# Performance work log

Hardware: AMD Instinct MI355X
Metric: run time of the kernel (lower is better)

## Reference

```python
import jax, jax.numpy as jnp
import numpy as np

N = 50000          # nodes
E = 1600000        # edges (avg degree 32)
D_MODEL = 128      # input == output dim
HEADS = 4
D_HEAD = D_MODEL // HEADS
N_LAYERS = 3


def _edge_softmax(scores, dst, n):
    # scores: [E, H]; softmax over edges sharing the same destination node
    m = jax.ops.segment_max(scores, dst, num_segments=n)          # [N, H]
    m = jnp.where(jnp.isfinite(m), m, 0.0)                        # empty segments -> -inf guard
    ex = jnp.exp(scores - m[dst])                                 # [E, H]
    denom = jax.ops.segment_sum(ex, dst, num_segments=n)          # [N, H]
    return ex / (denom[dst] + 1e-9)


def _gt_layer(h, src, dst, Wq, Wk, Wv, Wo):
    # h: [N, D]; one multi-head graph-attention (graph transformer) layer
    n = h.shape[0]
    q = (h @ Wq).reshape(n, HEADS, D_HEAD)
    k = (h @ Wk).reshape(n, HEADS, D_HEAD)
    v = (h @ Wv).reshape(n, HEADS, D_HEAD)
    scale = 1.0 / np.sqrt(D_HEAD).astype(np.float32)
    scores = jnp.einsum('ehd,ehd->eh', q[dst], k[src]) * scale    # [E, H]
    alpha = _edge_softmax(scores, dst, n)                         # [E, H]
    agg = jax.ops.segment_sum(alpha[:, :, None] * v[src], dst, num_segments=n)  # [N, H, Dh]
    return agg.reshape(n, D_MODEL) @ Wo


def setup_inputs() -> dict:
    key = jax.random.key(0)
    ks = jax.random.split(key, 16)
    s = 1.0 / np.sqrt(D_MODEL)
    inp = {
        'X':    jax.random.normal(ks[0], (N, 1), jnp.float32),
        'Seed': jax.random.uniform(ks[1], (N, 1), jnp.float32),
        'D':    jax.random.uniform(ks[2], (N, 1), jnp.float32),
        'C':    jax.random.uniform(ks[3], (N, 1), jnp.float32),
        'edge_src': jax.random.randint(ks[4], (E,), 0, N, jnp.int32),
        'edge_dst': jax.random.randint(ks[5], (E,), 0, N, jnp.int32),
        # scalar -> d_model embeddings (Linear(1, d, bias=False))
        'W_seed': jax.random.normal(ks[6], (1, D_MODEL), jnp.float32),
        'W_deg':  jax.random.normal(ks[7], (1, D_MODEL), jnp.float32),
        'W_clu':  jax.random.normal(ks[8], (1, D_MODEL), jnp.float32),
        # 3 graph-transformer layers
        'Wq': jax.random.normal(ks[9],  (N_LAYERS, D_MODEL, D_MODEL), jnp.float32) * s,
        'Wk': jax.random.normal(ks[10], (N_LAYERS, D_MODEL, D_MODEL), jnp.float32) * s,
        'Wv': jax.random.normal(ks[11], (N_LAYERS, D_MODEL, D_MODEL), jnp.float32) * s,
        'Wo': jax.random.normal(ks[12], (N_LAYERS, D_MODEL, D_MODEL), jnp.float32) * s,
        # MLP head: Linear(d,d)+ReLU, Linear(d,1)
        'W1': jax.random.normal(ks[13], (D_MODEL, D_MODEL), jnp.float32) * s,
        'b1': jnp.zeros((D_MODEL,), jnp.float32),
        'W2': jax.random.normal(ks[14], (D_MODEL, 1), jnp.float32) * s,
        'b2': jnp.zeros((1,), jnp.float32),
    }
    return inp


def reference(X, Seed, D, C, edge_src, edge_dst,
              W_seed, W_deg, W_clu, Wq, Wk, Wv, Wo, W1, b1, W2, b2):
    # faithful to original: raw X [N,1] broadcast-added to the embeddings
    h = X + Seed @ W_seed + D @ W_deg + C @ W_clu                 # [N, D_MODEL]
    for i in range(N_LAYERS):
        h = _gt_layer(h, edge_src, edge_dst, Wq[i], Wk[i], Wv[i], Wo[i])
    z = jax.nn.relu(h @ W1 + b1)
    return z @ W2 + b2                                            # [N, 1]
```

## Files before the change

### kernel.cpp

```cpp
#include <hip/hip_runtime.h>
#include <math.h>

#define DM 128
#define HEADS 4
#define DH 32
#define WSTRIDE 16384

typedef _Float16 f16x8 __attribute__((ext_vector_type(8)));
typedef _Float16 f16x4 __attribute__((ext_vector_type(4)));
typedef _Float16 f16x2 __attribute__((ext_vector_type(2)));
typedef float f32x4v __attribute__((ext_vector_type(4)));

__device__ __forceinline__ float dpp_xor1_add(float x) {
    int r = __builtin_amdgcn_update_dpp(0, __builtin_bit_cast(int, x), 0xB1, 0xf, 0xf, true);
    return x + __builtin_bit_cast(float, r);
}
__device__ __forceinline__ float dpp_xor2_add(float x) {
    int r = __builtin_amdgcn_update_dpp(0, __builtin_bit_cast(int, x), 0x4E, 0xf, 0xf, true);
    return x + __builtin_bit_cast(float, r);
}
__device__ __forceinline__ uint32_t pkh(float x, float y) {
    f16x2 h = {(_Float16)x, (_Float16)y};
    return __builtin_bit_cast(uint32_t, h);
}

__global__ void count_kernel(const int* __restrict__ edst, int* __restrict__ deg, int E) {
    int e = blockIdx.x * blockDim.x + threadIdx.x;
    if (e < E) atomicAdd(&deg[edst[e]], 1);
}

__global__ void scan1_kernel(const int* __restrict__ in, int* __restrict__ outv,
                             int* __restrict__ bsums, int n) {
    __shared__ int s[256];
    int t = threadIdx.x;
    int i = blockIdx.x * 256 + t;
    int v = (i < n) ? in[i] : 0;
    s[t] = v;
    __syncthreads();
    for (int off = 1; off < 256; off <<= 1) {
        int x = (t >= off) ? s[t - off] : 0;
        __syncthreads();
        s[t] += x;
        __syncthreads();
    }
    if (i < n) outv[i] = s[t];
    if (t == 255) bsums[blockIdx.x] = s[255];
}

__global__ void scan2_kernel(int* __restrict__ bsums, int nb) {
    __shared__ int s[256];
    int t = threadIdx.x;
    int v = (t < nb) ? bsums[t] : 0;
    s[t] = v;
    __syncthreads();
    for (int off = 1; off < 256; off <<= 1) {
        int x = (t >= off) ? s[t - off] : 0;
        __syncthreads();
        s[t] += x;
        __syncthreads();
    }
    if (t < nb) bsums[t] = s[t];
}

__global__ void scan3_kernel(const int* __restrict__ outv, const int* __restrict__ bsums,
                             int* __restrict__ ptr, int n) {
    int i = blockIdx.x * 256 + threadIdx.x;
    if (i == 0) ptr[0] = 0;
    if (i < n) {
        int add = (blockIdx.x > 0) ? bsums[blockIdx.x - 1] : 0;
        ptr[i + 1] = outv[i] + add;
    }
}

__global__ void scatter_kernel(const int* __restrict__ esrc, const int* __restrict__ edst,
                               const int* __restrict__ ptr, int* __restrict__ fill,
                               int* __restrict__ out, int E) {
    int e = blockIdx.x * blockDim.x + threadIdx.x;
    if (e >= E) return;
    int d = edst[e];
    int pos = ptr[d] + atomicAdd(&fill[d], 1);
    out[pos] = esrc[e];
}

__global__ void prepack_kernel(const float* __restrict__ Wq, const float* __restrict__ Wk,
                               const float* __restrict__ Wv, const float* __restrict__ Wo,
                               const float* __restrict__ W1, _Float16* __restrict__ W16) {
    int m = blockIdx.z;
    const float* W;
    if (m < 3)       W = Wq + (size_t)m * DM * DM;
    else if (m < 6)  W = Wk + (size_t)(m - 3) * DM * DM;
    else if (m < 9)  W = Wv + (size_t)(m - 6) * DM * DM;
    else if (m < 12) W = Wo + (size_t)(m - 9) * DM * DM;
    else             W = W1;
    int kb = blockIdx.x, nb = blockIdx.y, l = threadIdx.x;
    int kbase = kb * 32 + (l >> 4) * 8;
    int c = nb * 16 + (l & 15);
    f16x8 v;
#pragma unroll
    for (int j = 0; j < 8; j++) v[j] = (_Float16)W[(kbase + j) * DM + c];
    *reinterpret_cast<f16x8*>(W16 + (size_t)m * WSTRIDE + ((kb * 8 + nb) * 64 + l) * 8) = v;
}

__device__ __forceinline__ void tile_gemm(const _Float16* __restrict__ sRow,
                                          const _Float16* __restrict__ W16, int lg, int l,
                                          f32x4v acc[8]) {
#pragma unroll
    for (int nb = 0; nb < 8; nb++) acc[nb] = (f32x4v){0.f, 0.f, 0.f, 0.f};
#pragma unroll
    for (int kb = 0; kb < 4; kb++) {
        f16x8 a = *reinterpret_cast<const f16x8*>(sRow + kb * 32 + lg * 8);
#pragma unroll
        for (int nb = 0; nb < 8; nb++) {
            f16x8 b = *reinterpret_cast<const f16x8*>(&W16[((kb * 8 + nb) * 64 + l) * 8]);
            acc[nb] = __builtin_amdgcn_mfma_f32_16x16x32_f16(a, b, acc[nb], 0, 0, 0);
        }
    }
}

__device__ __forceinline__ void qkv_store(const _Float16* __restrict__ sH, int rowb, int lr,
                                          int lg, int l, int row0, int n,
                                          const _Float16* __restrict__ Wq16,
                                          const _Float16* __restrict__ Wk16,
                                          const _Float16* __restrict__ Wv16,
                                          _Float16* __restrict__ Qo,
                                          _Float16* __restrict__ KVo) {
    const _Float16* sRow = sH + (rowb + lr) * 136;
    f32x4v acc[8];
    tile_gemm(sRow, Wq16, lg, l, acc);
#pragma unroll
    for (int nb = 0; nb < 8; nb++)
#pragma unroll
        for (int i = 0; i < 4; i++) {
            int r = row0 + rowb + lg * 4 + i;
            if (r < n) Qo[(size_t)r * DM + nb * 16 + lr] = (_Float16)acc[nb][i];
        }
    tile_gemm(sRow, Wk16, lg, l, acc);
#pragma unroll
    for (int nb = 0; nb < 8; nb++)
#pragma unroll
        for (int i = 0; i < 4; i++) {
            int r = row0 + rowb + lg * 4 + i;
            if (r < n) KVo[(size_t)r * 256 + nb * 16 + lr] = (_Float16)acc[nb][i];
        }
    tile_gemm(sRow, Wv16, lg, l, acc);
#pragma unroll
    for (int nb = 0; nb < 8; nb++)
#pragma unroll
        for (int i = 0; i < 4; i++) {
            int r = row0 + rowb + lg * 4 + i;
            if (r < n) KVo[(size_t)r * 256 + 128 + nb * 16 + lr] = (_Float16)acc[nb][i];
        }
}

__global__ __launch_bounds__(256) void fused_embed_qkv_kernel(
    const float* __restrict__ X, const float* __restrict__ Seed,
    const float* __restrict__ Dg, const float* __restrict__ Cl,
    const float* __restrict__ Wseed, const float* __restrict__ Wdeg,
    const float* __restrict__ Wclu,
    const _Float16* __restrict__ Wq16, const _Float16* __restrict__ Wk16,
    const _Float16* __restrict__ Wv16,
    _Float16* __restrict__ Qo, _Float16* __restrict__ KVo, int n) {
    __shared__ _Float16 sH[64 * 136];
    int t = threadIdx.x;
    int row0 = blockIdx.x * 64;
    {
        int row = t >> 2, qt = t & 3;
        int gr = min(row0 + row, n - 1);
        float x = X[gr], sd = Seed[gr], dg = Dg[gr], cl = Cl[gr];
#pragma unroll
        for (int j = 0; j < 8; j++) {
            int c4 = qt * 32 + j * 4;
            float4 ws = *reinterpret_cast<const float4*>(Wseed + c4);
            float4 wd = *reinterpret_cast<const float4*>(Wdeg + c4);
            float4 wc = *reinterpret_cast<const float4*>(Wclu + c4);
            f16x4 h;
            h[0] = (_Float16)(x + sd * ws.x + dg * wd.x + cl * wc.x);
            h[1] = (_Float16)(x + sd * ws.y + dg * wd.y + cl * wc.y);
            h[2] = (_Float16)(x + sd * ws.z + dg * wd.z + cl * wc.z);
            h[3] = (_Float16)(x + sd * ws.w + dg * wd.w + cl * wc.w);
            *reinterpret_cast<f16x4*>(&sH[row * 136 + c4]) = h;
        }
    }
    __syncthreads();
    int w = t >> 6, l = t & 63;
    qkv_store(sH, w * 16, l & 15, l >> 4, l, row0, n, Wq16, Wk16, Wv16, Qo, KVo);
}

__global__ __launch_bounds__(256) void fused_wo_qkv_kernel(
    const _Float16* __restrict__ Ain, const _Float16* __restrict__ Wo16,
    const _Float16* __restrict__ Wq16, const _Float16* __restrict__ Wk16,
    const _Float16* __restrict__ Wv16,
    _Float16* __restrict__ Qo, _Float16* __restrict__ KVo, int n) {
    __shared__ _Float16 sA[64 * 136];
    __shared__ _Float16 sH[64 * 136];
    int t = threadIdx.x;
    int row0 = blockIdx.x * 64;
#pragma unroll
    for (int p = 0; p < 4; p++) {
        int f = p * 256 + t;
        int r = f >> 4, c8 = (f & 15) * 8;
        int gr = min(row0 + r, n - 1);
        *reinterpret_cast<uint4*>(&sA[r * 136 + c8]) =
            *reinterpret_cast<const uint4*>(Ain + (size_t)gr * DM + c8);
    }
    __syncthreads();
    int w = t >> 6, l = t & 63;
    int lr = l & 15, lg = l >> 4;
    int rowb = w * 16;
    f32x4v acc[8];
    tile_gemm(sA + (rowb + lr) * 136, Wo16, lg, l, acc);
#pragma unroll
    for (int nb = 0; nb < 8; nb++)
#pragma unroll
        for (int i = 0; i < 4; i++)
            sH[(rowb + lg * 4 + i) * 136 + nb * 16 + lr] = (_Float16)acc[nb][i];
    __syncthreads();
    qkv_store(sH, rowb, lr, lg, l, row0, n, Wq16, Wk16, Wv16, Qo, KVo);
}

__global__ __launch_bounds__(256) void fused_wo_mlp_kernel(
    const _Float16* __restrict__ Ain, const _Float16* __restrict__ Wo16,
    const _Float16* __restrict__ W116, const float* __restrict__ b1,
    const float* __restrict__ W2, const float* __restrict__ b2,
    float* __restrict__ out, int n) {
    __shared__ _Float16 sA[64 * 136];
    __shared__ _Float16 sH[64 * 136];
    int t = threadIdx.x;
    int row0 = blockIdx.x * 64;
#pragma unroll
    for (int p = 0; p < 4; p++) {
        int f = p * 256 + t;
        int r = f >> 4, c8 = (f & 15) * 8;
        int gr = min(row0 + r, n - 1);
        *reinterpret_cast<uint4*>(&sA[r * 136 + c8]) =
            *reinterpret_cast<const uint4*>(Ain + (size_t)gr * DM + c8);
    }
    __syncthreads();
    int w = t >> 6, l = t & 63;
    int lr = l & 15, lg = l >> 4;
    int rowb = w * 16;
    f32x4v acc[8];
    tile_gemm(sA + (rowb + lr) * 136, Wo16, lg, l, acc);
#pragma unroll
    for (int nb = 0; nb < 8; nb++)
#pragma unroll
        for (int i = 0; i < 4; i++)
            sH[(rowb + lg * 4 + i) * 136 + nb * 16 + lr] = (_Float16)acc[nb][i];
    __syncthreads();
    tile_gemm(sH + (rowb + lr) * 136, W116, lg, l, acc);
    float part[4] = {0.f, 0.f, 0.f, 0.f};
#pragma unroll
    for (int nb = 0; nb < 8; nb++) {
        int c = nb * 16 + lr;
        float b1v = b1[c];
        float w2v = W2[c];
#pragma unroll
        for (int i = 0; i < 4; i++) {
            float z = fmaxf(acc[nb][i] + b1v, 0.f);
            part[i] += z * w2v;
        }
    }
    float b2v = b2[0];
#pragma unroll
    for (int i = 0; i < 4; i++) {
        part[i] += __shfl_xor(part[i], 1, 64);
        part[i] += __shfl_xor(part[i], 2, 64);
        part[i] += __shfl_xor(part[i], 4, 64);
        part[i] += __shfl_xor(part[i], 8, 64);
        int r = row0 + rowb + lg * 4 + i;
        if (lr == 0 && r < n) out[r] = part[i] + b2v;
    }
}

__global__ __launch_bounds__(256) void attn_kernel(const _Float16* __restrict__ Q,
                                                   const uint32_t* __restrict__ KV,
                                                   const int* __restrict__ ptr,
                                                   const int* __restrict__ esrc,
                                                   _Float16* __restrict__ AGG, int n) {
    int wv = threadIdx.x >> 6;
    int lane = threadIdx.x & 63;
    int node = blockIdx.x * 4 + wv;
    if (node >= n) return;
    int e0 = ptr[node], e1 = ptr[node + 1];
    int q4 = lane >> 4;
    int w = lane & 15;
    _Float16* outbase = AGG + (size_t)node * DM + 8 * w;
    if (e0 >= e1) {
        if (lane < 16) *reinterpret_cast<uint4*>(outbase) = make_uint4(0, 0, 0, 0);
        return;
    }
    const float scale = 0.17677669529663687f * 1.4426950408889634f;
    uint4 qv = *reinterpret_cast<const uint4*>(Q + (size_t)node * DM + 8 * w);
    f16x2 qh0 = __builtin_bit_cast(f16x2, qv.x);
    f16x2 qh1 = __builtin_bit_cast(f16x2, qv.y);
    f16x2 qh2 = __builtin_bit_cast(f16x2, qv.z);
    f16x2 qh3 = __builtin_bit_cast(f16x2, qv.w);

    float m = -1e30f, s = 0.f;
    float a0 = 0.f, a1 = 0.f, a2 = 0.f, a3 = 0.f, a4 = 0.f, a5 = 0.f, a6 = 0.f, a7 = 0.f;

    int last = e1 - 1;
    int niter = (e1 - e0 + 3) >> 2;
    int niter2 = (niter + 1) >> 1;

    const uint32_t* kvw = KV + w * 4;

    uint4 k0, v0, k1, v1;
    {
        int i0 = esrc[min(e0 + q4, last)];
        const uint32_t* r0 = kvw + (size_t)i0 * 128;
        k0 = *reinterpret_cast<const uint4*>(r0);
        v0 = *reinterpret_cast<const uint4*>(r0 + 64);
        int i1 = esrc[min(e0 + 4 + q4, last)];
        const uint32_t* r1 = kvw + (size_t)i1 * 128;
        k1 = *reinterpret_cast<const uint4*>(r1);
        v1 = *reinterpret_cast<const uint4*>(r1 + 64);
    }
    int idx2 = esrc[min(e0 + 8 + q4, last)];

#define APROC(kc, vc, bidx)                                                            \
    {                                                                                  \
        float p = __builtin_amdgcn_fdot2(qh0, __builtin_bit_cast(f16x2, (kc).x), 0.f, false); \
        p = __builtin_amdgcn_fdot2(qh1, __builtin_bit_cast(f16x2, (kc).y), p, false);  \
        p = __builtin_amdgcn_fdot2(qh2, __builtin_bit_cast(f16x2, (kc).z), p, false);  \
        p = __builtin_amdgcn_fdot2(qh3, __builtin_bit_cast(f16x2, (kc).w), p, false);  \
        p = dpp_xor1_add(p);                                                           \
        p = dpp_xor2_add(p);                                                           \
        p *= scale;                                                                    \
        p = ((bidx) < e1) ? p : -3.0e38f;                                              \
        float diff = p - m;                                                            \
        if (__any(diff > 8.f)) {                                                       \
            float mn = fmaxf(m, p);                                                    \
            float dd = exp2f(m - mn);                                                  \
            s *= dd;                                                                   \
            a0 *= dd; a1 *= dd; a2 *= dd; a3 *= dd;                                    \
            a4 *= dd; a5 *= dd; a6 *= dd; a7 *= dd;                                    \
            m = mn;                                                                    \
            diff = p - m;                                                              \
        }                                                                              \
        float wg = exp2f(diff);                                                        \
        s += wg;                                                                       \
        f16x2 vh0 = __builtin_bit_cast(f16x2, (vc).x);                                 \
        f16x2 vh1 = __builtin_bit_cast(f16x2, (vc).y);                                 \
        f16x2 vh2 = __builtin_bit_cast(f16x2, (vc).z);                                 \
        f16x2 vh3 = __builtin_bit_cast(f16x2, (vc).w);                                 \
        a0 += wg * (float)vh0[0]; a1 += wg * (float)vh0[1];                            \
        a2 += wg * (float)vh1[0]; a3 += wg * (float)vh1[1];                            \
        a4 += wg * (float)vh2[0]; a5 += wg * (float)vh2[1];                            \
        a6 += wg * (float)vh3[0]; a7 += wg * (float)vh3[1];                            \
    }

    int b = e0 + q4;
    for (int it = 0; it < niter2; it++) {
        {
            uint4 kc = k0, vc = v0;
            const uint32_t* r = kvw + (size_t)idx2 * 128;
            k0 = *reinterpret_cast<const uint4*>(r);
            v0 = *reinterpret_cast<const uint4*>(r + 64);
            idx2 = esrc[min(b + 12, last)];
            APROC(kc, vc, b);
            b += 4;
        }
        {
            uint4 kc = k1, vc = v1;
            const uint32_t* r = kvw + (size_t)idx2 * 128;
            k1 = *reinterpret_cast<const uint4*>(r);
            v1 = *reinterpret_cast<const uint4*>(r + 64);
            idx2 = esrc[min(b + 12, last)];
            APROC(kc, vc, b);
            b += 4;
        }
    }
#undef APROC

#pragma unroll
    for (int off = 16; off <= 32; off <<= 1) {
        float m2 = __shfl_xor(m, off, 64);
        float s2 = __shfl_xor(s, off, 64);
        float b0 = __shfl_xor(a0, off, 64), b1 = __shfl_xor(a1, off, 64);
        float b2 = __shfl_xor(a2, off, 64), b3 = __shfl_xor(a3, off, 64);
        float b4 = __shfl_xor(a4, off, 64), b5 = __shfl_xor(a5, off, 64);
        float b6 = __shfl_xor(a6, off, 64), b7 = __shfl_xor(a7, off, 64);
        float mF = fmaxf(m, m2);
        float d1 = exp2f(m - mF), d2 = exp2f(m2 - mF);
        s = s * d1 + s2 * d2;
        a0 = a0 * d1 + b0 * d2; a1 = a1 * d1 + b1 * d2;
        a2 = a2 * d1 + b2 * d2; a3 = a3 * d1 + b3 * d2;
        a4 = a4 * d1 + b4 * d2; a5 = a5 * d1 + b5 * d2;
        a6 = a6 * d1 + b6 * d2; a7 = a7 * d1 + b7 * d2;
        m = mF;
    }

    float inv = 1.f / (s + 1e-9f);
    if (lane < 16) {
        uint4 o;
        o.x = pkh(a0 * inv, a1 * inv);
        o.y = pkh(a2 * inv, a3 * inv);
        o.z = pkh(a4 * inv, a5 * inv);
        o.w = pkh(a6 * inv, a7 * inv);
        *reinterpret_cast<uint4*>(outbase) = o;
    }
}

extern "C" void kernel_launch(void* const* d_in, const int* in_sizes, int n_in,
                              void* d_out, int out_size, void* d_ws, size_t ws_size,
                              hipStream_t stream) {
    const float* X    = (const float*)d_in[0];
    const float* Seed = (const float*)d_in[1];
    const float* Dg   = (const float*)d_in[2];
    const float* Cl   = (const float*)d_in[3];
    const int* esrc   = (const int*)d_in[4];
    const int* edst   = (const int*)d_in[5];
    const float* Wseed = (const float*)d_in[6];
    const float* Wdeg  = (const float*)d_in[7];
    const float* Wclu  = (const float*)d_in[8];
    const float* Wq = (const float*)d_in[9];
    const float* Wk = (const float*)d_in[10];
    const float* Wv = (const float*)d_in[11];
    const float* Wo = (const float*)d_in[12];
    const float* W1 = (const float*)d_in[13];
    const float* b1 = (const float*)d_in[14];
    const float* W2 = (const float*)d_in[15];
    const float* b2 = (const float*)d_in[16];
    float* out = (float*)d_out;

    int n = in_sizes[0];
    int E = in_sizes[4];

    char* p = (char*)d_ws;
    auto alloc = [&](size_t bytes) {
        void* r = (void*)p;
        p += (bytes + 255) & ~(size_t)255;
        return r;
    };
    _Float16* qbuf = (_Float16*)alloc((size_t)n * DM * 2);
    _Float16* abuf = (_Float16*)alloc((size_t)n * DM * 2);
    unsigned short* kvbuf = (unsigned short*)alloc((size_t)n * 256 * 2);
    _Float16* W16 = (_Float16*)alloc((size_t)13 * WSTRIDE * 2);
    int* deg    = (int*)alloc((size_t)n * 4);
    int* ptr    = (int*)alloc((size_t)(n + 1) * 4);
    int* ptrtmp = (int*)alloc((size_t)n * 4);
    int* bsums  = (int*)alloc(1024);
    int* fill   = (int*)alloc((size_t)n * 4);
    int* esrcs  = (int*)alloc((size_t)E * 4);
    (void)ws_size; (void)n_in; (void)out_size;

    hipMemsetAsync(deg, 0, (size_t)n * 4, stream);
    hipMemsetAsync(fill, 0, (size_t)n * 4, stream);

    int nb = (n + 255) / 256;
    count_kernel<<<(E + 255) / 256, 256, 0, stream>>>(edst, deg, E);
    scan1_kernel<<<nb, 256, 0, stream>>>(deg, ptrtmp, bsums, n);
    scan2_kernel<<<1, 256, 0, stream>>>(bsums, nb);
    scan3_kernel<<<nb, 256, 0, stream>>>(ptrtmp, bsums, ptr, n);
    scatter_kernel<<<(E + 255) / 256, 256, 0, stream>>>(esrc, edst, ptr, fill, esrcs, E);

    prepack_kernel<<<dim3(4, 8, 13), 64, 0, stream>>>(Wq, Wk, Wv, Wo, W1, W16);

    int ggrid = (n + 63) / 64;
    int agrid = (n + 3) / 4;
    const _Float16* KVc = (const _Float16*)kvbuf;

    fused_embed_qkv_kernel<<<ggrid, 256, 0, stream>>>(
        X, Seed, Dg, Cl, Wseed, Wdeg, Wclu,
        W16 + (size_t)0 * WSTRIDE, W16 + (size_t)3 * WSTRIDE, W16 + (size_t)6 * WSTRIDE,
        qbuf, (_Float16*)kvbuf, n);
    attn_kernel<<<agrid, 256, 0, stream>>>(qbuf, (const uint32_t*)KVc, ptr, esrcs, abuf, n);
    for (int i = 0; i < 2; i++) {
        fused_wo_qkv_kernel<<<ggrid, 256, 0, stream>>>(
            abuf, W16 + (size_t)(9 + i) * WSTRIDE,
            W16 + (size_t)(1 + i) * WSTRIDE, W16 + (size_t)(4 + i) * WSTRIDE,
            W16 + (size_t)(7 + i) * WSTRIDE, qbuf, (_Float16*)kvbuf, n);
        attn_kernel<<<agrid, 256, 0, stream>>>(qbuf, (const uint32_t*)KVc, ptr, esrcs, abuf, n);
    }
    fused_wo_mlp_kernel<<<ggrid, 256, 0, stream>>>(
        abuf, W16 + (size_t)11 * WSTRIDE, W16 + (size_t)12 * WSTRIDE, b1, W2, b2, out, n);
}
```

Before: 670.7 us.

## Transpose MFMA operands for vector stores, deepen attention prefetch, simplify CSR scatter

```diff
diff --git a/kernel.cpp b/kernel.cpp
--- a/kernel.cpp
+++ b/kernel.cpp
@@ -2,8 +2,6 @@
 #include <math.h>
 
 #define DM 128
-#define HEADS 4
-#define DH 32
 #define WSTRIDE 16384
 
 typedef _Float16 f16x8 __attribute__((ext_vector_type(8)));
@@ -63,22 +61,27 @@
 }
 
 __global__ void scan3_kernel(const int* __restrict__ outv, const int* __restrict__ bsums,
-                             int* __restrict__ ptr, int n) {
+                             int* __restrict__ ptr, int* __restrict__ cur, int n) {
     int i = blockIdx.x * 256 + threadIdx.x;
     if (i == 0) ptr[0] = 0;
     if (i < n) {
         int add = (blockIdx.x > 0) ? bsums[blockIdx.x - 1] : 0;
-        ptr[i + 1] = outv[i] + add;
-    }
+        int incl = outv[i] + add;
+        ptr[i + 1] = incl;
+        cur[i] = incl - ((i < n) ? (outv[i] - ((i & 255) ? outv[i] - outv[i] : 0)) : 0);
+    }
+}
+
+__global__ void initcur_kernel(const int* __restrict__ ptr, int* __restrict__ cur, int n) {
+    int i = blockIdx.x * blockDim.x + threadIdx.x;
+    if (i < n) cur[i] = ptr[i];
 }
 
 __global__ void scatter_kernel(const int* __restrict__ esrc, const int* __restrict__ edst,
-                               const int* __restrict__ ptr, int* __restrict__ fill,
-                               int* __restrict__ out, int E) {
+                               int* __restrict__ cur, int* __restrict__ out, int E) {
     int e = blockIdx.x * blockDim.x + threadIdx.x;
     if (e >= E) return;
-    int d = edst[e];
-    int pos = ptr[d] + atomicAdd(&fill[d], 1);
+    int pos = atomicAdd(&cur[edst[e]], 1);
     out[pos] = esrc[e];
 }
 
@@ -101,9 +104,9 @@
     *reinterpret_cast<f16x8*>(W16 + (size_t)m * WSTRIDE + ((kb * 8 + nb) * 64 + l) * 8) = v;
 }
 
-__device__ __forceinline__ void tile_gemm(const _Float16* __restrict__ sRow,
-                                          const _Float16* __restrict__ W16, int lg, int l,
-                                          f32x4v acc[8]) {
+__device__ __forceinline__ void tile_gemm_T(const _Float16* __restrict__ sRow,
+                                            const _Float16* __restrict__ W16, int lg, int l,
+                                            f32x4v acc[8]) {
 #pragma unroll
     for (int nb = 0; nb < 8; nb++) acc[nb] = (f32x4v){0.f, 0.f, 0.f, 0.f};
 #pragma unroll
@@ -112,44 +115,45 @@
 #pragma unroll
         for (int nb = 0; nb < 8; nb++) {
             f16x8 b = *reinterpret_cast<const f16x8*>(&W16[((kb * 8 + nb) * 64 + l) * 8]);
-            acc[nb] = __builtin_amdgcn_mfma_f32_16x16x32_f16(a, b, acc[nb], 0, 0, 0);
+            acc[nb] = __builtin_amdgcn_mfma_f32_16x16x32_f16(b, a, acc[nb], 0, 0, 0);
         }
     }
 }
 
-__device__ __forceinline__ void qkv_store(const _Float16* __restrict__ sH, int rowb, int lr,
-                                          int lg, int l, int row0, int n,
-                                          const _Float16* __restrict__ Wq16,
-                                          const _Float16* __restrict__ Wk16,
-                                          const _Float16* __restrict__ Wv16,
-                                          _Float16* __restrict__ Qo,
-                                          _Float16* __restrict__ KVo) {
-    const _Float16* sRow = sH + (rowb + lr) * 136;
+__device__ __forceinline__ f16x4 pk4(const f32x4v a) {
+    f16x4 h = {(_Float16)a[0], (_Float16)a[1], (_Float16)a[2], (_Float16)a[3]};
+    return h;
+}
+
+__device__ __forceinline__ void qkv_store_T(const _Float16* __restrict__ sRow, int lr, int lg,
+                                            int l, int rowb, int row0, int n,
+                                            const _Float16* __restrict__ Wq16,
+                                            const _Float16* __restrict__ Wk16,
+                                            const _Float16* __restrict__ Wv16,
+                                            _Float16* __restrict__ Qo,
+                                            _Float16* __restrict__ KVo) {
+    int r = row0 + rowb + lr;
+    bool ok = (r < n);
     f32x4v acc[8];
-    tile_gemm(sRow, Wq16, lg, l, acc);
-#pragma unroll
-    for (int nb = 0; nb < 8; nb++)
-#pragma unroll
-        for (int i = 0; i < 4; i++) {
-            int r = row0 + rowb + lg * 4 + i;
-            if (r < n) Qo[(size_t)r * DM + nb * 16 + lr] = (_Float16)acc[nb][i];
-        }
-    tile_gemm(sRow, Wk16, lg, l, acc);
-#pragma unroll
-    for (int nb = 0; nb < 8; nb++)
-#pragma unroll
-        for (int i = 0; i < 4; i++) {
-            int r = row0 + rowb + lg * 4 + i;
-            if (r < n) KVo[(size_t)r * 256 + nb * 16 + lr] = (_Float16)acc[nb][i];
-        }
-    tile_gemm(sRow, Wv16, lg, l, acc);
-#pragma unroll
-    for (int nb = 0; nb < 8; nb++)
-#pragma unroll
-        for (int i = 0; i < 4; i++) {
-            int r = row0 + rowb + lg * 4 + i;
-            if (r < n) KVo[(size_t)r * 256 + 128 + nb * 16 + lr] = (_Float16)acc[nb][i];
-        }
+    tile_gemm_T(sRow, Wq16, lg, l, acc);
+    if (ok) {
+#pragma unroll
+        for (int nb = 0; nb < 8; nb++)
+            *reinterpret_cast<f16x4*>(Qo + (size_t)r * DM + nb * 16 + lg * 4) = pk4(acc[nb]);
+    }
+    tile_gemm_T(sRow, Wk16, lg, l, acc);
+    if (ok) {
+#pragma unroll
+        for (int nb = 0; nb < 8; nb++)
+            *reinterpret_cast<f16x4*>(KVo + (size_t)r * 256 + nb * 16 + lg * 4) = pk4(acc[nb]);
+    }
+    tile_gemm_T(sRow, Wv16, lg, l, acc);
+    if (ok) {
+#pragma unroll
+        for (int nb = 0; nb < 8; nb++)
+            *reinterpret_cast<f16x4*>(KVo + (size_t)r * 256 + 128 + nb * 16 + lg * 4) =
+                pk4(acc[nb]);
+    }
 }
 
 __global__ __launch_bounds__(256) void fused_embed_qkv_kernel(
@@ -183,7 +187,8 @@
     }
     __syncthreads();
     int w = t >> 6, l = t & 63;
-    qkv_store(sH, w * 16, l & 15, l >> 4, l, row0, n, Wq16, Wk16, Wv16, Qo, KVo);
+    int lr = l & 15, lg = l >> 4;
+    qkv_store_T(sH + (w * 16 + lr) * 136, lr, lg, l, w * 16, row0, n, Wq16, Wk16, Wv16, Qo, KVo);
 }
 
 __global__ __launch_bounds__(256) void fused_wo_qkv_kernel(
@@ -208,14 +213,12 @@
     int lr = l & 15, lg = l >> 4;
     int rowb = w * 16;
     f32x4v acc[8];
-    tile_gemm(sA + (rowb + lr) * 136, Wo16, lg, l, acc);
+    tile_gemm_T(sA + (rowb + lr) * 136, Wo16, lg, l, acc);
 #pragma unroll
     for (int nb = 0; nb < 8; nb++)
-#pragma unroll
-        for (int i = 0; i < 4; i++)
-            sH[(rowb + lg * 4 + i) * 136 + nb * 16 + lr] = (_Float16)acc[nb][i];
-    __syncthreads();
-    qkv_store(sH, rowb, lr, lg, l, row0, n, Wq16, Wk16, Wv16, Qo, KVo);
+        *reinterpret_cast<f16x4*>(&sH[(rowb + lr) * 136 + nb * 16 + lg * 4]) = pk4(acc[nb]);
+    __syncthreads();
+    qkv_store_T(sH + (rowb + lr) * 136, lr, lg, l, rowb, row0, n, Wq16, Wk16, Wv16, Qo, KVo);
 }
 
 __global__ __launch_bounds__(256) void fused_wo_mlp_kernel(
@@ -240,36 +243,25 @@
     int lr = l & 15, lg = l >> 4;
     int rowb = w * 16;
     f32x4v acc[8];
-    tile_gemm(sA + (rowb + lr) * 136, Wo16, lg, l, acc);
+    tile_gemm_T(sA + (rowb + lr) * 136, Wo16, lg, l, acc);
 #pragma unroll
     for (int nb = 0; nb < 8; nb++)
-#pragma unroll
-        for (int i = 0; i < 4; i++)
-            sH[(rowb + lg * 4 + i) * 136 + nb * 16 + lr] = (_Float16)acc[nb][i];
-    __syncthreads();
-    tile_gemm(sH + (rowb + lr) * 136, W116, lg, l, acc);
-    float part[4] = {0.f, 0.f, 0.f, 0.f};
+        *reinterpret_cast<f16x4*>(&sH[(rowb + lr) * 136 + nb * 16 + lg * 4]) = pk4(acc[nb]);
+    __syncthreads();
+    tile_gemm_T(sH + (rowb + lr) * 136, W116, lg, l, acc);
+    float part = 0.f;
 #pragma unroll
     for (int nb = 0; nb < 8; nb++) {
-        int c = nb * 16 + lr;
-        float b1v = b1[c];
-        float w2v = W2[c];
 #pragma unroll
         for (int i = 0; i < 4; i++) {
-            float z = fmaxf(acc[nb][i] + b1v, 0.f);
-            part[i] += z * w2v;
+            int c = nb * 16 + lg * 4 + i;
+            part += fmaxf(acc[nb][i] + b1[c], 0.f) * W2[c];
         }
     }
-    float b2v = b2[0];
-#pragma unroll
-    for (int i = 0; i < 4; i++) {
-        part[i] += __shfl_xor(part[i], 1, 64);
-        part[i] += __shfl_xor(part[i], 2, 64);
-        part[i] += __shfl_xor(part[i], 4, 64);
-        part[i] += __shfl_xor(part[i], 8, 64);
-        int r = row0 + rowb + lg * 4 + i;
-        if (lr == 0 && r < n) out[r] = part[i] + b2v;
-    }
+    part += __shfl_xor(part, 16, 64);
+    part += __shfl_xor(part, 32, 64);
+    int r = row0 + rowb + lr;
+    if (lg == 0 && r < n) out[r] = part + b2[0];
 }
 
 __global__ __launch_bounds__(256) void attn_kernel(const _Float16* __restrict__ Q,
@@ -300,23 +292,27 @@
     float a0 = 0.f, a1 = 0.f, a2 = 0.f, a3 = 0.f, a4 = 0.f, a5 = 0.f, a6 = 0.f, a7 = 0.f;
 
     int last = e1 - 1;
-    int niter = (e1 - e0 + 3) >> 2;
-    int niter2 = (niter + 1) >> 1;
+    int S = (e1 - e0 + 3) >> 2;
+    int loops = (S + 3) >> 2;
 
     const uint32_t* kvw = KV + w * 4;
 
-    uint4 k0, v0, k1, v1;
+    uint4 k0, v0, k1, v1, k2, v2, k3, v3;
     {
-        int i0 = esrc[min(e0 + q4, last)];
-        const uint32_t* r0 = kvw + (size_t)i0 * 128;
+        const uint32_t* r0 = kvw + (size_t)esrc[min(e0 + q4, last)] * 128;
         k0 = *reinterpret_cast<const uint4*>(r0);
         v0 = *reinterpret_cast<const uint4*>(r0 + 64);
-        int i1 = esrc[min(e0 + 4 + q4, last)];
-        const uint32_t* r1 = kvw + (size_t)i1 * 128;
+        const uint32_t* r1 = kvw + (size_t)esrc[min(e0 + 4 + q4, last)] * 128;
         k1 = *reinterpret_cast<const uint4*>(r1);
         v1 = *reinterpret_cast<const uint4*>(r1 + 64);
-    }
-    int idx2 = esrc[min(e0 + 8 + q4, last)];
+        const uint32_t* r2 = kvw + (size_t)esrc[min(e0 + 8 + q4, last)] * 128;
+        k2 = *reinterpret_cast<const uint4*>(r2);
+        v2 = *reinterpret_cast<const uint4*>(r2 + 64);
+        const uint32_t* r3 = kvw + (size_t)esrc[min(e0 + 12 + q4, last)] * 128;
+        k3 = *reinterpret_cast<const uint4*>(r3);
+        v3 = *reinterpret_cast<const uint4*>(r3 + 64);
+    }
+    int idxn = esrc[min(e0 + 16 + q4, last)];
 
 #define APROC(kc, vc, bidx)                                                            \
     {                                                                                  \
@@ -350,27 +346,25 @@
         a6 += wg * (float)vh3[0]; a7 += wg * (float)vh3[1];                            \
     }
 
+#define SUBSTEP(kx, vx)                                                                \
+    {                                                                                  \
+        uint4 kc = kx, vc = vx;                                                        \
+        const uint32_t* r = kvw + (size_t)idxn * 128;                                  \
+        kx = *reinterpret_cast<const uint4*>(r);                                       \
+        vx = *reinterpret_cast<const uint4*>(r + 64);                                  \
+        idxn = esrc[min(b + 20, last)];                                                \
+        APROC(kc, vc, b);                                                              \
+        b += 4;                                                                        \
+    }
+
     int b = e0 + q4;
-    for (int it = 0; it < niter2; it++) {
-        {
-            uint4 kc = k0, vc = v0;
-            const uint32_t* r = kvw + (size_t)idx2 * 128;
-            k0 = *reinterpret_cast<const uint4*>(r);
-            v0 = *reinterpret_cast<const uint4*>(r + 64);
-            idx2 = esrc[min(b + 12, last)];
-            APROC(kc, vc, b);
-            b += 4;
-        }
-        {
-            uint4 kc = k1, vc = v1;
-            const uint32_t* r = kvw + (size_t)idx2 * 128;
-            k1 = *reinterpret_cast<const uint4*>(r);
-            v1 = *reinterpret_cast<const uint4*>(r + 64);
-            idx2 = esrc[min(b + 12, last)];
-            APROC(kc, vc, b);
-            b += 4;
-        }
-    }
+    for (int it = 0; it < loops; it++) {
+        SUBSTEP(k0, v0);
+        SUBSTEP(k1, v1);
+        SUBSTEP(k2, v2);
+        SUBSTEP(k3, v3);
+    }
+#undef SUBSTEP
 #undef APROC
 
 #pragma unroll
@@ -441,37 +435,37 @@
     int* ptr    = (int*)alloc((size_t)(n + 1) * 4);
     int* ptrtmp = (int*)alloc((size_t)n * 4);
     int* bsums  = (int*)alloc(1024);
-    int* fill   = (int*)alloc((size_t)n * 4);
+    int* cur    = (int*)alloc((size_t)n * 4);
     int* esrcs  = (int*)alloc((size_t)E * 4);
     (void)ws_size; (void)n_in; (void)out_size;
 
     hipMemsetAsync(deg, 0, (size_t)n * 4, stream);
-    hipMemsetAsync(fill, 0, (size_t)n * 4, stream);
 
     int nb = (n + 255) / 256;
     count_kernel<<<(E + 255) / 256, 256, 0, stream>>>(edst, deg, E);
     scan1_kernel<<<nb, 256, 0, stream>>>(deg, ptrtmp, bsums, n);
     scan2_kernel<<<1, 256, 0, stream>>>(bsums, nb);
-    scan3_kernel<<<nb, 256, 0, stream>>>(ptrtmp, bsums, ptr, n);
-    scatter_kernel<<<(E + 255) / 256, 256, 0, stream>>>(esrc, edst, ptr, fill, esrcs, E);
+    scan3_kernel<<<nb, 256, 0, stream>>>(ptrtmp, bsums, ptr, cur, n);
+    initcur_kernel<<<nb, 256, 0, stream>>>(ptr, cur, n);
+    scatter_kernel<<<(E + 255) / 256, 256, 0, stream>>>(esrc, edst, cur, esrcs, E);
 
     prepack_kernel<<<dim3(4, 8, 13), 64, 0, stream>>>(Wq, Wk, Wv, Wo, W1, W16);
 
     int ggrid = (n + 63) / 64;
     int agrid = (n + 3) / 4;
-    const _Float16* KVc = (const _Float16*)kvbuf;
+    const uint32_t* KVc = (const uint32_t*)kvbuf;
 
     fused_embed_qkv_kernel<<<ggrid, 256, 0, stream>>>(
         X, Seed, Dg, Cl, Wseed, Wdeg, Wclu,
         W16 + (size_t)0 * WSTRIDE, W16 + (size_t)3 * WSTRIDE, W16 + (size_t)6 * WSTRIDE,
         qbuf, (_Float16*)kvbuf, n);
-    attn_kernel<<<agrid, 256, 0, stream>>>(qbuf, (const uint32_t*)KVc, ptr, esrcs, abuf, n);
+    attn_kernel<<<agrid, 256, 0, stream>>>(qbuf, KVc, ptr, esrcs, abuf, n);
     for (int i = 0; i < 2; i++) {
         fused_wo_qkv_kernel<<<ggrid, 256, 0, stream>>>(
             abuf, W16 + (size_t)(9 + i) * WSTRIDE,
             W16 + (size_t)(1 + i) * WSTRIDE, W16 + (size_t)(4 + i) * WSTRIDE,
             W16 + (size_t)(7 + i) * WSTRIDE, qbuf, (_Float16*)kvbuf, n);
-        attn_kernel<<<agrid, 256, 0, stream>>>(qbuf, (const uint32_t*)KVc, ptr, esrcs, abuf, n);
+        attn_kernel<<<agrid, 256, 0, stream>>>(qbuf, KVc, ptr, esrcs, abuf, n);
     }
     fused_wo_mlp_kernel<<<ggrid, 256, 0, stream>>>(
         abuf, W16 + (size_t)11 * WSTRIDE, W16 + (size_t)12 * WSTRIDE, b1, W2, b2, out, n);
```

Result: slower. 722.1 us (+7.7%).
